# Kernel tuning notes

Measured on AMD Instinct MI355X. Metric: run time of the kernel, lower is better.

## Reference

```python
import jax, jax.numpy as jnp
import numpy as np

N = 16384
E = 262144
HID = 128
NFILT = 128
NGAUSS = 50
NINTER = 6
CUTOFF = 10.0
NUMZ = 100
LOG2 = 0.6931471805599453


def ssp(x):
    # ShiftedSoftplus
    return jax.nn.softplus(x) - LOG2


def setup_inputs() -> dict:
    key = jax.random.key(0)
    ks = jax.random.split(key, 20)
    z = jax.random.randint(ks[0], (N,), 0, NUMZ)
    pos = jax.random.uniform(ks[1], (N, 3), dtype=jnp.float32) * 5.0  # box side 5 -> all pairs < cutoff
    edge_index = jax.random.randint(ks[2], (2, E), 0, N)
    s = lambda k, shape, fan: jax.random.normal(k, shape, dtype=jnp.float32) / np.sqrt(fan)
    params = dict(
        emb=s(ks[3], (NUMZ, HID), 1.0),
        Wf1=s(ks[4], (NINTER, NGAUSS, NFILT), NGAUSS), bf1=jnp.zeros((NINTER, NFILT), jnp.float32),
        Wf2=s(ks[5], (NINTER, NFILT, NFILT), NFILT), bf2=jnp.zeros((NINTER, NFILT), jnp.float32),
        Wl1=s(ks[6], (NINTER, HID, NFILT), HID),
        Wl2=s(ks[7], (NINTER, NFILT, HID), NFILT), bl2=jnp.zeros((NINTER, HID), jnp.float32),
        Wl=s(ks[8], (NINTER, HID, HID), HID), bl=jnp.zeros((NINTER, HID), jnp.float32),
        Wo1=s(ks[9], (HID, HID // 2), HID), bo1=jnp.zeros((HID // 2,), jnp.float32),
        Wo2=s(ks[10], (HID // 2, 1), HID // 2), bo2=jnp.zeros((1,), jnp.float32),
    )
    return dict(z=z, pos=pos, edge_index=edge_index, **params)


def reference(z, pos, edge_index, emb, Wf1, bf1, Wf2, bf2, Wl1, Wl2, bl2, Wl, bl, Wo1, bo1, Wo2, bo2):
    src, dst = edge_index[0], edge_index[1]
    # edge distances and Gaussian smearing
    d = jnp.linalg.norm(pos[src] - pos[dst], axis=-1)          # [E]
    offset = jnp.linspace(0.0, CUTOFF, NGAUSS, dtype=jnp.float32)
    coeff = -0.5 / (offset[1] - offset[0]) ** 2
    ea = jnp.exp(coeff * (d[:, None] - offset) ** 2)            # [E, NGAUSS]
    C = 0.5 * (jnp.cos(d * (np.pi / CUTOFF)) + 1.0)             # cosine cutoff [E]

    h = emb[z]                                                  # [N, HID]
    for i in range(NINTER):
        # continuous-filter weights
        Wfilt = (ssp(ea @ Wf1[i] + bf1[i]) @ Wf2[i] + bf2[i]) * C[:, None]  # [E, NFILT]
        x = h @ Wl1[i]                                          # lin1, no bias [N, NFILT]
        msg = x[src] * Wfilt                                    # gather + filter
        agg = jax.ops.segment_sum(msg, dst, num_segments=N)     # scatter-sum [N, NFILT]
        x = ssp(agg @ Wl2[i] + bl2[i]) @ Wl[i] + bl[i]          # lin2 -> ssp -> lin
        h = h + x

    h = ssp(h @ Wo1 + bo1) @ Wo2 + bo2                          # [N, 1] per-atom energy
    out = jnp.sum(h, axis=0, keepdims=True)                     # 'add' readout, single graph -> [1, 1]
    return jax.nn.relu(out)
```

## Files before the change

kernel.cpp:

```cpp
#include <hip/hip_runtime.h>
#include <math.h>

#define NATOM 16384
#define NEDGE 262144
#define HID 128
#define NG 50
#define NI 6

typedef _Float16 h8_t __attribute__((ext_vector_type(8)));
typedef _Float16 h4_t __attribute__((ext_vector_type(4)));
typedef float    f4_t __attribute__((ext_vector_type(4)));

__device__ __forceinline__ float ssp_f(float v) {
    float e = __expf(-fabsf(v));
    return fmaxf(v, 0.0f) + __logf(1.0f + e) - 0.69314718055994531f;
}

__global__ void fill0(float* __restrict__ p, int n4) {
    int i = blockIdx.x * 256 + threadIdx.x;
    if (i < n4) ((float4*)p)[i] = make_float4(0.f, 0.f, 0.f, 0.f);
}

__global__ void hist_k(const int* __restrict__ ei, int* __restrict__ cnt) {
    int e = blockIdx.x * 256 + threadIdx.x;
    if (e < NEDGE) atomicAdd(&cnt[ei[NEDGE + e]], 1);
}

__global__ void scan_k(const int* __restrict__ cnt, int* __restrict__ offs) {
    __shared__ int part[256];
    int t = threadIdx.x;
    int base = t * 64;
    int s = 0;
    for (int i = 0; i < 64; ++i) s += cnt[base + i];
    part[t] = s;
    __syncthreads();
    for (int off = 1; off < 256; off <<= 1) {
        int v = (t >= off) ? part[t - off] : 0;
        __syncthreads();
        part[t] += v;
        __syncthreads();
    }
    int r = part[t] - s;
    for (int i = 0; i < 64; ++i) { offs[base + i] = r; r += cnt[base + i]; }
    if (t == 255) offs[NATOM] = r;
}

__global__ void scatter_k(const int* __restrict__ ei, const int* __restrict__ offs,
                          int* __restrict__ cnt, int* __restrict__ sSrc, int* __restrict__ sDst) {
    int e = blockIdx.x * 256 + threadIdx.x;
    if (e >= NEDGE) return;
    int d = ei[NEDGE + e];
    int r = atomicAdd(&cnt[d], 1);
    int j = offs[d] + r;
    sSrc[j] = ei[e];
    sDst[j] = d;
}

__global__ void edge_pre(const float* __restrict__ pos,
                         const int* __restrict__ sSrc, const int* __restrict__ sDst,
                         _Float16* __restrict__ eaH, _Float16* __restrict__ eaL,
                         float* __restrict__ Cb) {
    int j = blockIdx.x * 256 + threadIdx.x;
    if (j >= NEDGE) return;
    int s = sSrc[j], dd = sDst[j];
    float dx = pos[3*s]   - pos[3*dd];
    float dy = pos[3*s+1] - pos[3*dd+1];
    float dz = pos[3*s+2] - pos[3*dd+2];
    float d = sqrtf(dx*dx + dy*dy + dz*dz);
    Cb[j] = 0.5f * (cosf(d * 0.31415926535897931f) + 1.0f);
    const float delta = 10.0f / 49.0f;
    const float coeff = -0.5f / (delta * delta);
    #pragma unroll
    for (int gq = 0; gq < 8; ++gq) {
        h8_t hv, lv;
        #pragma unroll
        for (int r = 0; r < 8; ++r) {
            int g = gq * 8 + r;
            float v = 0.0f;
            if (g < NG) { float u = d - (float)g * delta; v = __expf(coeff * u * u); }
            _Float16 hh = (_Float16)v;
            hv[r] = hh;
            lv[r] = (_Float16)(v - (float)hh);
        }
        *(h8_t*)&eaH[(size_t)j * 64 + gq * 8] = hv;
        *(h8_t*)&eaL[(size_t)j * 64 + gq * 8] = lv;
    }
}

__global__ void wprep(const float* __restrict__ Wf1, const float* __restrict__ Wf2,
                      const float* __restrict__ Wl1, const float* __restrict__ Wl2,
                      const float* __restrict__ Wl,
                      _Float16* __restrict__ w1h, _Float16* __restrict__ w1l,
                      _Float16* __restrict__ w2h, _Float16* __restrict__ w2l,
                      _Float16* __restrict__ wnh, _Float16* __restrict__ wnl) {
    int idx = blockIdx.x * 256 + threadIdx.x;
    const int S1 = NI * 128 * 64, S2 = NI * 128 * 128;
    if (idx < S1) {
        int i = idx >> 13, r = idx & 8191, fo = r >> 6, k = r & 63;
        float v = (k < NG) ? Wf1[(size_t)i * NG * 128 + k * 128 + fo] : 0.0f;
        _Float16 hh = (_Float16)v;
        w1h[idx] = hh; w1l[idx] = (_Float16)(v - (float)hh);
        return;
    }
    idx -= S1;
    if (idx < S2) {
        int i = idx >> 14, r = idx & 16383, fo = r >> 7, k = r & 127;
        float v = Wf2[(size_t)i * 128 * 128 + k * 128 + fo];
        _Float16 hh = (_Float16)v;
        w2h[idx] = hh; w2l[idx] = (_Float16)(v - (float)hh);
        return;
    }
    idx -= S2;
    if (idx < 3 * S2) {
        int mi = idx >> 14;
        int r = idx & 16383, fo = r >> 7, k = r & 127;
        int m = mi / NI, i = mi % NI;
        const float* W = (m == 0) ? Wl1 : (m == 1) ? Wl2 : Wl;
        float v = W[(size_t)i * 128 * 128 + k * 128 + fo];
        _Float16 hh = (_Float16)v;
        wnh[idx] = hh; wnl[idx] = (_Float16)(v - (float)hh);
    }
}

__global__ void embed_k(const int* __restrict__ z, const float* __restrict__ emb,
                        float* __restrict__ h) {
    int tid = blockIdx.x * 256 + threadIdx.x;
    int n = tid >> 7, f = tid & 127;
    h[tid] = emb[z[n] * HID + f];
}

__launch_bounds__(256)
__global__ void gemm_node_mfma(const float* __restrict__ A,
                               const _Float16* __restrict__ wth, const _Float16* __restrict__ wtl,
                               float* __restrict__ Cout) {
    __shared__ _Float16 aH[64 * 136];
    __shared__ _Float16 aL[64 * 136];
    int t = threadIdx.x;
    int mb = blockIdx.x * 64;
    #pragma unroll
    for (int j = 0; j < 8; ++j) {
        int idx = t + j * 256;
        int row = idx >> 5, c4 = idx & 31;
        f4_t v = *(const f4_t*)&A[(size_t)(mb + row) * HID + c4 * 4];
        h4_t hh, ll;
        #pragma unroll
        for (int r = 0; r < 4; ++r) {
            _Float16 hx = (_Float16)v[r];
            hh[r] = hx; ll[r] = (_Float16)(v[r] - (float)hx);
        }
        *(h4_t*)&aH[row * 136 + c4 * 4] = hh;
        *(h4_t*)&aL[row * 136 + c4 * 4] = ll;
    }
    __syncthreads();

    int wv = t >> 6, lane = t & 63, l15 = lane & 15, quad = lane >> 4;
    f4_t acc[2][4];
    #pragma unroll
    for (int m = 0; m < 2; ++m)
        #pragma unroll
        for (int n = 0; n < 4; ++n) acc[m][n] = (f4_t)0.0f;

    for (int kc = 0; kc < 4; ++kc) {
        int k0 = kc * 32 + quad * 8;
        h8_t a_h[2], a_l[2];
        #pragma unroll
        for (int m = 0; m < 2; ++m) {
            int fr = wv * 32 + m * 16 + l15;
            a_h[m] = *(const h8_t*)&wth[fr * 128 + k0];
            a_l[m] = *(const h8_t*)&wtl[fr * 128 + k0];
        }
        #pragma unroll
        for (int n = 0; n < 4; ++n) {
            int er = n * 16 + l15;
            h8_t b_h = *(const h8_t*)&aH[er * 136 + k0];
            h8_t b_l = *(const h8_t*)&aL[er * 136 + k0];
            #pragma unroll
            for (int m = 0; m < 2; ++m) {
                acc[m][n] = __builtin_amdgcn_mfma_f32_16x16x32_f16(a_h[m], b_h, acc[m][n], 0, 0, 0);
                acc[m][n] = __builtin_amdgcn_mfma_f32_16x16x32_f16(a_h[m], b_l, acc[m][n], 0, 0, 0);
                acc[m][n] = __builtin_amdgcn_mfma_f32_16x16x32_f16(a_l[m], b_h, acc[m][n], 0, 0, 0);
            }
        }
    }

    #pragma unroll
    for (int n = 0; n < 4; ++n) {
        int el = n * 16 + l15;
        size_t row = (size_t)(mb + el);
        #pragma unroll
        for (int m = 0; m < 2; ++m) {
            int fb = wv * 32 + m * 16 + quad * 4;
            f4_t o;
            #pragma unroll
            for (int r = 0; r < 4; ++r) o[r] = acc[m][n][r];
            *(f4_t*)&Cout[row * 128 + fb] = o;
        }
    }
}

__launch_bounds__(256)
__global__ void gemm_node3(const float* __restrict__ agg,
                           const _Float16* __restrict__ w2th, const _Float16* __restrict__ w2tl,
                           const _Float16* __restrict__ wlth, const _Float16* __restrict__ wltl,
                           const _Float16* __restrict__ w1nh, const _Float16* __restrict__ w1nl,
                           const float* __restrict__ bl2, const float* __restrict__ bl,
                           float* __restrict__ h, float* __restrict__ x) {
    __shared__ _Float16 aH[64 * 136];
    __shared__ _Float16 aL[64 * 136];
    int t = threadIdx.x;
    int mb = blockIdx.x * 64;
    #pragma unroll
    for (int j = 0; j < 8; ++j) {
        int idx = t + j * 256;
        int row = idx >> 5, c4 = idx & 31;
        f4_t v = *(const f4_t*)&agg[(size_t)(mb + row) * HID + c4 * 4];
        h4_t hh, ll;
        #pragma unroll
        for (int r = 0; r < 4; ++r) {
            _Float16 hx = (_Float16)v[r];
            hh[r] = hx; ll[r] = (_Float16)(v[r] - (float)hx);
        }
        *(h4_t*)&aH[row * 136 + c4 * 4] = hh;
        *(h4_t*)&aL[row * 136 + c4 * 4] = ll;
    }
    __syncthreads();

    int wv = t >> 6, lane = t & 63, l15 = lane & 15, quad = lane >> 4;
    int fq = wv * 32 + quad * 4;
    f4_t acc[2][4];

    #pragma unroll
    for (int m = 0; m < 2; ++m)
        #pragma unroll
        for (int n = 0; n < 4; ++n) acc[m][n] = (f4_t)0.0f;
    for (int kc = 0; kc < 4; ++kc) {
        int k0 = kc * 32 + quad * 8;
        h8_t a_h[2], a_l[2];
        #pragma unroll
        for (int m = 0; m < 2; ++m) {
            int fr = wv * 32 + m * 16 + l15;
            a_h[m] = *(const h8_t*)&w2th[fr * 128 + k0];
            a_l[m] = *(const h8_t*)&w2tl[fr * 128 + k0];
        }
        #pragma unroll
        for (int n = 0; n < 4; ++n) {
            int er = n * 16 + l15;
            h8_t b_h = *(const h8_t*)&aH[er * 136 + k0];
            h8_t b_l = *(const h8_t*)&aL[er * 136 + k0];
            #pragma unroll
            for (int m = 0; m < 2; ++m) {
                acc[m][n] = __builtin_amdgcn_mfma_f32_16x16x32_f16(a_h[m], b_h, acc[m][n], 0, 0, 0);
                acc[m][n] = __builtin_amdgcn_mfma_f32_16x16x32_f16(a_h[m], b_l, acc[m][n], 0, 0, 0);
                acc[m][n] = __builtin_amdgcn_mfma_f32_16x16x32_f16(a_l[m], b_h, acc[m][n], 0, 0, 0);
            }
        }
    }
    f4_t b2v[2];
    b2v[0] = *(const f4_t*)&bl2[fq]; b2v[1] = *(const f4_t*)&bl2[fq + 16];
    __syncthreads();

    #pragma unroll
    for (int m = 0; m < 2; ++m)
        #pragma unroll
        for (int n = 0; n < 4; ++n) {
            int el = n * 16 + l15;
            int fb = wv * 32 + m * 16 + quad * 4;
            h4_t hh, ll;
            #pragma unroll
            for (int r = 0; r < 4; ++r) {
                float sv = ssp_f(acc[m][n][r] + b2v[m][r]);
                _Float16 hx = (_Float16)sv;
                hh[r] = hx;
                ll[r] = (_Float16)(sv - (float)hx);
            }
            *(h4_t*)&aH[el * 136 + fb] = hh;
            *(h4_t*)&aL[el * 136 + fb] = ll;
        }
    __syncthreads();

    #pragma unroll
    for (int m = 0; m < 2; ++m)
        #pragma unroll
        for (int n = 0; n < 4; ++n) acc[m][n] = (f4_t)0.0f;
    for (int kc = 0; kc < 4; ++kc) {
        int k0 = kc * 32 + quad * 8;
        h8_t a_h[2], a_l[2];
        #pragma unroll
        for (int m = 0; m < 2; ++m) {
            int fr = wv * 32 + m * 16 + l15;
            a_h[m] = *(const h8_t*)&wlth[fr * 128 + k0];
            a_l[m] = *(const h8_t*)&wltl[fr * 128 + k0];
        }
        #pragma unroll
        for (int n = 0; n < 4; ++n) {
            int er = n * 16 + l15;
            h8_t b_h = *(const h8_t*)&aH[er * 136 + k0];
            h8_t b_l = *(const h8_t*)&aL[er * 136 + k0];
            #pragma unroll
            for (int m = 0; m < 2; ++m) {
                acc[m][n] = __builtin_amdgcn_mfma_f32_16x16x32_f16(a_h[m], b_h, acc[m][n], 0, 0, 0);
                acc[m][n] = __builtin_amdgcn_mfma_f32_16x16x32_f16(a_h[m], b_l, acc[m][n], 0, 0, 0);
                acc[m][n] = __builtin_amdgcn_mfma_f32_16x16x32_f16(a_l[m], b_h, acc[m][n], 0, 0, 0);
            }
        }
    }
    f4_t blv[2];
    blv[0] = *(const f4_t*)&bl[fq]; blv[1] = *(const f4_t*)&bl[fq + 16];
    __syncthreads();

    #pragma unroll
    for (int n = 0; n < 4; ++n) {
        int el = n * 16 + l15;
        size_t row = (size_t)(mb + el);
        #pragma unroll
        for (int m = 0; m < 2; ++m) {
            int fb = wv * 32 + m * 16 + quad * 4;
            f4_t hv = *(const f4_t*)&h[row * 128 + fb];
            f4_t o;
            h4_t hh, ll;
            #pragma unroll
            for (int r = 0; r < 4; ++r) {
                o[r] = hv[r] + acc[m][n][r] + blv[m][r];
                _Float16 hx = (_Float16)o[r];
                hh[r] = hx; ll[r] = (_Float16)(o[r] - (float)hx);
            }
            *(f4_t*)&h[row * 128 + fb] = o;
            *(h4_t*)&aH[el * 136 + fb] = hh;
            *(h4_t*)&aL[el * 136 + fb] = ll;
        }
    }
    if (!w1nh) return;
    __syncthreads();

    #pragma unroll
    for (int m = 0; m < 2; ++m)
        #pragma unroll
        for (int n = 0; n < 4; ++n) acc[m][n] = (f4_t)0.0f;
    for (int kc = 0; kc < 4; ++kc) {
        int k0 = kc * 32 + quad * 8;
        h8_t a_h[2], a_l[2];
        #pragma unroll
        for (int m = 0; m < 2; ++m) {
            int fr = wv * 32 + m * 16 + l15;
            a_h[m] = *(const h8_t*)&w1nh[fr * 128 + k0];
            a_l[m] = *(const h8_t*)&w1nl[fr * 128 + k0];
        }
        #pragma unroll
        for (int n = 0; n < 4; ++n) {
            int er = n * 16 + l15;
            h8_t b_h = *(const h8_t*)&aH[er * 136 + k0];
            h8_t b_l = *(const h8_t*)&aL[er * 136 + k0];
            #pragma unroll
            for (int m = 0; m < 2; ++m) {
                acc[m][n] = __builtin_amdgcn_mfma_f32_16x16x32_f16(a_h[m], b_h, acc[m][n], 0, 0, 0);
                acc[m][n] = __builtin_amdgcn_mfma_f32_16x16x32_f16(a_h[m], b_l, acc[m][n], 0, 0, 0);
                acc[m][n] = __builtin_amdgcn_mfma_f32_16x16x32_f16(a_l[m], b_h, acc[m][n], 0, 0, 0);
            }
        }
    }
    #pragma unroll
    for (int n = 0; n < 4; ++n) {
        int el = n * 16 + l15;
        size_t row = (size_t)(mb + el);
        #pragma unroll
        for (int m = 0; m < 2; ++m) {
            int fb = wv * 32 + m * 16 + quad * 4;
            f4_t o;
            #pragma unroll
            for (int r = 0; r < 4; ++r) o[r] = acc[m][n][r];
            *(f4_t*)&x[row * 128 + fb] = o;
        }
    }
}

#define T1_LDW 136
#define MROW 132
#define EF_TPB 4

__launch_bounds__(256, 2)
__global__ void edge_filter(const float* __restrict__ x, float* __restrict__ agg,
                            const int* __restrict__ sSrc, const int* __restrict__ sDst,
                            const float* __restrict__ Cb,
                            const _Float16* __restrict__ eaH, const _Float16* __restrict__ eaL,
                            const _Float16* __restrict__ w1h, const _Float16* __restrict__ w1l,
                            const _Float16* __restrict__ w2h, const _Float16* __restrict__ w2l,
                            const float* __restrict__ bf1, const float* __restrict__ bf2) {
    __shared__ __align__(16) _Float16 eaHs[64 * 72];
    __shared__ __align__(16) _Float16 eaLs[64 * 72];
    __shared__ __align__(16) unsigned char t1mem[34816];
    __shared__ float cL[64];
    __shared__ int dstl[64];
    __shared__ int srcl[64];

    _Float16* t1H = (_Float16*)t1mem;
    _Float16* t1L = (_Float16*)(t1mem + 17408);
    float*    msg = (float*)t1mem;

    int t = threadIdx.x;
    int wv = t >> 6, lane = t & 63;
    int l15 = lane & 15, quad = lane >> 4;
    int tile0 = blockIdx.x * EF_TPB;

    h8_t w1fh[2][2], w1fl[2][2], w2fh[4][2], w2fl[4][2];
    #pragma unroll
    for (int kc = 0; kc < 2; ++kc) {
        int k0 = kc * 32 + quad * 8;
        #pragma unroll
        for (int m = 0; m < 2; ++m) {
            int fr = wv * 32 + m * 16 + l15;
            w1fh[kc][m] = *(const h8_t*)&w1h[fr * 64 + k0];
            w1fl[kc][m] = *(const h8_t*)&w1l[fr * 64 + k0];
        }
    }
    #pragma unroll
    for (int kc = 0; kc < 4; ++kc) {
        int k0 = kc * 32 + quad * 8;
        #pragma unroll
        for (int m = 0; m < 2; ++m) {
            int fr = wv * 32 + m * 16 + l15;
            w2fh[kc][m] = *(const h8_t*)&w2h[fr * 128 + k0];
            w2fl[kc][m] = *(const h8_t*)&w2l[fr * 128 + k0];
        }
    }
    int fq = wv * 32 + quad * 4;
    f4_t b1v[2], b2v[2];
    b1v[0] = *(const f4_t*)&bf1[fq];  b1v[1] = *(const f4_t*)&bf1[fq + 16];
    b2v[0] = *(const f4_t*)&bf2[fq];  b2v[1] = *(const f4_t*)&bf2[fq + 16];

    {
        int eb = tile0 * 64;
        if (t < 64) {
            srcl[t] = sSrc[eb + t];
            dstl[t] = sDst[eb + t];
            cL[t]   = Cb[eb + t];
        }
        #pragma unroll
        for (int c = 0; c < 4; ++c) {
            int ch = t + c * 256;
            int pl = ch >> 9, rem = ch & 511, e = rem >> 3, ks = rem & 7;
            h8_t v = *(const h8_t*)((pl ? eaL : eaH) + (size_t)(eb + e) * 64 + ks * 8);
            *(h8_t*)((pl ? eaLs : eaHs) + e * 72 + ks * 8) = v;
        }
    }
    __syncthreads();

    for (int tt = 0; tt < EF_TPB; ++tt) {
        if (tt > 0) {
            __syncthreads();
            if (t < 64) {
                int e = (tile0 + tt) * 64 + t;
                srcl[t] = sSrc[e];
                dstl[t] = sDst[e];
                cL[t]   = Cb[e];
            }
        }
        bool pre = (tt < EF_TPB - 1);
        h8_t sreg[4];
        if (pre) {
            int ebn = (tile0 + tt + 1) * 64;
            #pragma unroll
            for (int c = 0; c < 4; ++c) {
                int ch = t + c * 256;
                int pl = ch >> 9, rem = ch & 511, e = rem >> 3, ks = rem & 7;
                sreg[c] = *(const h8_t*)((pl ? eaL : eaH) + (size_t)(ebn + e) * 64 + ks * 8);
            }
        }

        f4_t acc1[2][4];
        #pragma unroll
        for (int m = 0; m < 2; ++m)
            #pragma unroll
            for (int n = 0; n < 4; ++n) acc1[m][n] = (f4_t)0.0f;
        #pragma unroll
        for (int kc = 0; kc < 2; ++kc) {
            int k0 = kc * 32 + quad * 8;
            h8_t b_h[4], b_l[4];
            #pragma unroll
            for (int n = 0; n < 4; ++n) {
                int er = n * 16 + l15;
                b_h[n] = *(const h8_t*)&eaHs[er * 72 + k0];
                b_l[n] = *(const h8_t*)&eaLs[er * 72 + k0];
            }
            #pragma unroll
            for (int m = 0; m < 2; ++m)
                #pragma unroll
                for (int n = 0; n < 4; ++n) {
                    acc1[m][n] = __builtin_amdgcn_mfma_f32_16x16x32_f16(w1fh[kc][m], b_h[n], acc1[m][n], 0, 0, 0);
                    acc1[m][n] = __builtin_amdgcn_mfma_f32_16x16x32_f16(w1fh[kc][m], b_l[n], acc1[m][n], 0, 0, 0);
                    acc1[m][n] = __builtin_amdgcn_mfma_f32_16x16x32_f16(w1fl[kc][m], b_h[n], acc1[m][n], 0, 0, 0);
                }
        }

        #pragma unroll
        for (int m = 0; m < 2; ++m)
            #pragma unroll
            for (int n = 0; n < 4; ++n) {
                int el = n * 16 + l15;
                int fb = wv * 32 + m * 16 + quad * 4;
                h4_t hh, ll;
                #pragma unroll
                for (int r = 0; r < 4; ++r) {
                    float sv = ssp_f(acc1[m][n][r] + b1v[m][r]);
                    _Float16 hx = (_Float16)sv;
                    hh[r] = hx;
                    ll[r] = (_Float16)(sv - (float)hx);
                }
                *(h4_t*)&t1H[el * T1_LDW + fb] = hh;
                *(h4_t*)&t1L[el * T1_LDW + fb] = ll;
            }
        __syncthreads();

        if (pre) {
            #pragma unroll
            for (int c = 0; c < 4; ++c) {
                int ch = t + c * 256;
                int pl = ch >> 9, rem = ch & 511, e = rem >> 3, ks = rem & 7;
                *(h8_t*)((pl ? eaLs : eaHs) + e * 72 + ks * 8) = sreg[c];
            }
        }
        f4_t xr[4][2];
        #pragma unroll
        for (int n = 0; n < 4; ++n) {
            int el = n * 16 + l15;
            int s = srcl[el];
            #pragma unroll
            for (int m = 0; m < 2; ++m) {
                int fb = wv * 32 + m * 16 + quad * 4;
                xr[n][m] = *(const f4_t*)&x[(size_t)s * HID + fb];
            }
        }

        f4_t acc2[2][4];
        #pragma unroll
        for (int m = 0; m < 2; ++m)
            #pragma unroll
            for (int n = 0; n < 4; ++n) acc2[m][n] = (f4_t)0.0f;
        #pragma unroll
        for (int kc = 0; kc < 4; ++kc) {
            int k0 = kc * 32 + quad * 8;
            #pragma unroll
            for (int n = 0; n < 4; ++n) {
                int er = n * 16 + l15;
                h8_t b_h = *(const h8_t*)&t1H[er * T1_LDW + k0];
                h8_t b_l = *(const h8_t*)&t1L[er * T1_LDW + k0];
                #pragma unroll
                for (int m = 0; m < 2; ++m) {
                    acc2[m][n] = __builtin_amdgcn_mfma_f32_16x16x32_f16(w2fh[kc][m], b_h, acc2[m][n], 0, 0, 0);
                    acc2[m][n] = __builtin_amdgcn_mfma_f32_16x16x32_f16(w2fh[kc][m], b_l, acc2[m][n], 0, 0, 0);
                    acc2[m][n] = __builtin_amdgcn_mfma_f32_16x16x32_f16(w2fl[kc][m], b_h, acc2[m][n], 0, 0, 0);
                }
            }
        }
        __syncthreads();

        #pragma unroll
        for (int n = 0; n < 4; ++n) {
            int el = n * 16 + l15;
            float ce = cL[el];
            #pragma unroll
            for (int m = 0; m < 2; ++m) {
                int fb = wv * 32 + m * 16 + quad * 4;
                f4_t o;
                #pragma unroll
                for (int r = 0; r < 4; ++r)
                    o[r] = (acc2[m][n][r] + b2v[m][r]) * ce * xr[n][m][r];
                *(f4_t*)&msg[el * MROW + fb] = o;
            }
        }
        __syncthreads();

        int f = t & 127, hf = t >> 7;
        int ib = hf * 32;
        float run = 0.0f;
        int cur = dstl[ib];
        for (int i = ib; i < ib + 32; ++i) {
            int dnow = dstl[i];
            if (dnow != cur) {
                atomicAdd(&agg[(size_t)cur * HID + f], run);
                run = 0.0f;
                cur = dnow;
            }
            run += msg[i * MROW + f];
        }
        atomicAdd(&agg[(size_t)cur * HID + f], run);
    }
}

__launch_bounds__(256)
__global__ void readout1(const float* __restrict__ h, const float* __restrict__ Wo1,
                         const float* __restrict__ bo1, const float* __restrict__ Wo2,
                         const float* __restrict__ bo2, float* __restrict__ accum) {
    __shared__ float w1[128 * 64];
    __shared__ float part[4];
    int t = threadIdx.x;
    for (int i = t; i < 128 * 16; i += 256)
        ((float4*)w1)[i] = ((const float4*)Wo1)[i];
    __syncthreads();
    int f = t & 63, wv = t >> 6;
    float b = bo1[f], w2v = Wo2[f];
    float lsum = 0.0f;
    for (int a = 0; a < 16; ++a) {
        int n = blockIdx.x * 64 + wv * 16 + a;
        const float* hr = &h[(size_t)n * HID];
        float acc = b;
        #pragma unroll 16
        for (int k = 0; k < 128; ++k)
            acc = fmaf(hr[k], w1[k*64 + f], acc);
        lsum += ssp_f(acc) * w2v;
    }
    #pragma unroll
    for (int off = 32; off > 0; off >>= 1)
        lsum += __shfl_down(lsum, off, 64);
    if (f == 0) part[wv] = lsum;
    __syncthreads();
    if (t == 0)
        atomicAdd(accum, part[0] + part[1] + part[2] + part[3] + 64.0f * bo2[0]);
}

__global__ void readout2(const float* __restrict__ accum, float* __restrict__ out) {
    out[0] = fmaxf(accum[0], 0.0f);
}

extern "C" void kernel_launch(void* const* d_in, const int* in_sizes, int n_in,
                              void* d_out, int out_size, void* d_ws, size_t ws_size,
                              hipStream_t stream) {
    const int*   z   = (const int*)d_in[0];
    const float* pos = (const float*)d_in[1];
    const int*   ei  = (const int*)d_in[2];
    const float* emb = (const float*)d_in[3];
    const float* Wf1 = (const float*)d_in[4];
    const float* bf1 = (const float*)d_in[5];
    const float* Wf2 = (const float*)d_in[6];
    const float* bf2 = (const float*)d_in[7];
    const float* Wl1 = (const float*)d_in[8];
    const float* Wl2 = (const float*)d_in[9];
    const float* bl2 = (const float*)d_in[10];
    const float* Wl  = (const float*)d_in[11];
    const float* bl  = (const float*)d_in[12];
    const float* Wo1 = (const float*)d_in[13];
    const float* bo1 = (const float*)d_in[14];
    const float* Wo2 = (const float*)d_in[15];
    const float* bo2 = (const float*)d_in[16];
    float* out = (float*)d_out;

    _Float16* w1h = (_Float16*)d_ws;
    _Float16* w1l = w1h + NI * 8192;
    _Float16* w2h = w1l + NI * 8192;
    _Float16* w2l = w2h + NI * 16384;
    _Float16* wnh = w2l + NI * 16384;
    _Float16* wnl = wnh + 3 * NI * 16384;
    _Float16* eaH = wnl + 3 * NI * 16384;
    _Float16* eaL = eaH + (size_t)NEDGE * 64;
    float* Cb  = (float*)(eaL + (size_t)NEDGE * 64);
    float* h   = Cb + NEDGE;
    float* x   = h   + (size_t)NATOM * HID;
    float* agg = x   + (size_t)NATOM * HID;
    float* accum = agg + (size_t)NATOM * HID;
    int* cnt  = (int*)(accum + 4);
    int* offs = cnt + NATOM;
    int* sSrc = offs + NATOM + 4;
    int* sDst = sSrc + NEDGE;

    fill0<<<NATOM/4/256, 256, 0, stream>>>((float*)cnt, NATOM/4);
    hist_k<<<NEDGE/256, 256, 0, stream>>>(ei, cnt);
    scan_k<<<1, 256, 0, stream>>>(cnt, offs);
    fill0<<<NATOM/4/256, 256, 0, stream>>>((float*)cnt, NATOM/4);
    scatter_k<<<NEDGE/256, 256, 0, stream>>>(ei, offs, cnt, sSrc, sDst);

    edge_pre<<<NEDGE/256, 256, 0, stream>>>(pos, sSrc, sDst, eaH, eaL, Cb);
    wprep<<<(NI*8192 + NI*16384 + 3*NI*16384)/256, 256, 0, stream>>>(
        Wf1, Wf2, Wl1, Wl2, Wl, w1h, w1l, w2h, w2l, wnh, wnl);
    embed_k<<<(NATOM*HID)/256, 256, 0, stream>>>(z, emb, h);

    gemm_node_mfma<<<256, 256, 0, stream>>>(h, wnh + (size_t)0*16384,
        wnl + (size_t)0*16384, x);
    for (int i = 0; i < NI; ++i) {
        fill0<<<(NATOM*HID/4)/256, 256, 0, stream>>>(agg, NATOM*HID/4);
        edge_filter<<<NEDGE/64/EF_TPB, 256, 0, stream>>>(x, agg, sSrc, sDst, Cb, eaH, eaL,
            w1h + (size_t)i*8192, w1l + (size_t)i*8192,
            w2h + (size_t)i*16384, w2l + (size_t)i*16384,
            bf1 + i*HID, bf2 + i*HID);
        const _Float16* w1nh = (i < NI-1) ? wnh + (size_t)(i+1)*16384 : nullptr;
        const _Float16* w1nl = (i < NI-1) ? wnl + (size_t)(i+1)*16384 : nullptr;
        gemm_node3<<<256, 256, 0, stream>>>(agg,
            wnh + (size_t)(1*NI+i)*16384, wnl + (size_t)(1*NI+i)*16384,
            wnh + (size_t)(2*NI+i)*16384, wnl + (size_t)(2*NI+i)*16384,
            w1nh, w1nl, bl2 + i*HID, bl + i*HID, h, x);
    }
    fill0<<<1, 256, 0, stream>>>(accum, 1);
    readout1<<<NATOM/64, 256, 0, stream>>>(h, Wo1, bo1, Wo2, bo2, accum);
    readout2<<<1, 1, 0, stream>>>(accum, out);
}
```

Before: 791.3 us.

## Use single fp16 edge filter GEMMs, fp16 node features, and register-level segmented scatter

Drops the split hi/lo fp16 emulation of fp32 in the edge filter MLP, so each GEMM uses one MFMA per product instead of three. Node features x are now stored as fp16, halving the gather traffic. The scatter-sum moves from an LDS message buffer with a serial run-length loop to a wave-level segmented scan with shuffles, and edge indices now live in registers. LDS use shrinks and occupancy is raised to 3 blocks per SM. The cost is lower numerical precision in the filter weights and messages, which may break accuracy tolerance.

```diff
diff --git a/kernel.cpp b/kernel.cpp
--- a/kernel.cpp
+++ b/kernel.cpp
@@ -58,8 +58,7 @@
 
 __global__ void edge_pre(const float* __restrict__ pos,
                          const int* __restrict__ sSrc, const int* __restrict__ sDst,
-                         _Float16* __restrict__ eaH, _Float16* __restrict__ eaL,
-                         float* __restrict__ Cb) {
+                         _Float16* __restrict__ ea, float* __restrict__ Cb) {
     int j = blockIdx.x * 256 + threadIdx.x;
     if (j >= NEDGE) return;
     int s = sSrc[j], dd = sDst[j];
@@ -72,42 +71,35 @@
     const float coeff = -0.5f / (delta * delta);
     #pragma unroll
     for (int gq = 0; gq < 8; ++gq) {
-        h8_t hv, lv;
+        h8_t hv;
         #pragma unroll
         for (int r = 0; r < 8; ++r) {
             int g = gq * 8 + r;
             float v = 0.0f;
             if (g < NG) { float u = d - (float)g * delta; v = __expf(coeff * u * u); }
-            _Float16 hh = (_Float16)v;
-            hv[r] = hh;
-            lv[r] = (_Float16)(v - (float)hh);
-        }
-        *(h8_t*)&eaH[(size_t)j * 64 + gq * 8] = hv;
-        *(h8_t*)&eaL[(size_t)j * 64 + gq * 8] = lv;
+            hv[r] = (_Float16)v;
+        }
+        *(h8_t*)&ea[(size_t)j * 64 + gq * 8] = hv;
     }
 }
 
 __global__ void wprep(const float* __restrict__ Wf1, const float* __restrict__ Wf2,
                       const float* __restrict__ Wl1, const float* __restrict__ Wl2,
                       const float* __restrict__ Wl,
-                      _Float16* __restrict__ w1h, _Float16* __restrict__ w1l,
-                      _Float16* __restrict__ w2h, _Float16* __restrict__ w2l,
+                      _Float16* __restrict__ w1, _Float16* __restrict__ w2,
                       _Float16* __restrict__ wnh, _Float16* __restrict__ wnl) {
     int idx = blockIdx.x * 256 + threadIdx.x;
     const int S1 = NI * 128 * 64, S2 = NI * 128 * 128;
     if (idx < S1) {
         int i = idx >> 13, r = idx & 8191, fo = r >> 6, k = r & 63;
         float v = (k < NG) ? Wf1[(size_t)i * NG * 128 + k * 128 + fo] : 0.0f;
-        _Float16 hh = (_Float16)v;
-        w1h[idx] = hh; w1l[idx] = (_Float16)(v - (float)hh);
+        w1[idx] = (_Float16)v;
         return;
     }
     idx -= S1;
     if (idx < S2) {
         int i = idx >> 14, r = idx & 16383, fo = r >> 7, k = r & 127;
-        float v = Wf2[(size_t)i * 128 * 128 + k * 128 + fo];
-        _Float16 hh = (_Float16)v;
-        w2h[idx] = hh; w2l[idx] = (_Float16)(v - (float)hh);
+        w2[idx] = (_Float16)Wf2[(size_t)i * 128 * 128 + k * 128 + fo];
         return;
     }
     idx -= S2;
@@ -132,7 +124,7 @@
 __launch_bounds__(256)
 __global__ void gemm_node_mfma(const float* __restrict__ A,
                                const _Float16* __restrict__ wth, const _Float16* __restrict__ wtl,
-                               float* __restrict__ Cout) {
+                               _Float16* __restrict__ xh) {
     __shared__ _Float16 aH[64 * 136];
     __shared__ _Float16 aL[64 * 136];
     int t = threadIdx.x;
@@ -190,10 +182,10 @@
         #pragma unroll
         for (int m = 0; m < 2; ++m) {
             int fb = wv * 32 + m * 16 + quad * 4;
-            f4_t o;
-            #pragma unroll
-            for (int r = 0; r < 4; ++r) o[r] = acc[m][n][r];
-            *(f4_t*)&Cout[row * 128 + fb] = o;
+            h4_t o;
+            #pragma unroll
+            for (int r = 0; r < 4; ++r) o[r] = (_Float16)acc[m][n][r];
+            *(h4_t*)&xh[row * 128 + fb] = o;
         }
     }
 }
@@ -204,7 +196,7 @@
                            const _Float16* __restrict__ wlth, const _Float16* __restrict__ wltl,
                            const _Float16* __restrict__ w1nh, const _Float16* __restrict__ w1nl,
                            const float* __restrict__ bl2, const float* __restrict__ bl,
-                           float* __restrict__ h, float* __restrict__ x) {
+                           float* __restrict__ h, _Float16* __restrict__ xh) {
     __shared__ _Float16 aH[64 * 136];
     __shared__ _Float16 aL[64 * 136];
     int t = threadIdx.x;
@@ -365,51 +357,41 @@
         #pragma unroll
         for (int m = 0; m < 2; ++m) {
             int fb = wv * 32 + m * 16 + quad * 4;
-            f4_t o;
-            #pragma unroll
-            for (int r = 0; r < 4; ++r) o[r] = acc[m][n][r];
-            *(f4_t*)&x[row * 128 + fb] = o;
+            h4_t o;
+            #pragma unroll
+            for (int r = 0; r < 4; ++r) o[r] = (_Float16)acc[m][n][r];
+            *(h4_t*)&xh[row * 128 + fb] = o;
         }
     }
 }
 
 #define T1_LDW 136
-#define MROW 132
+#define EA_LDW 72
 #define EF_TPB 4
 
-__launch_bounds__(256, 2)
-__global__ void edge_filter(const float* __restrict__ x, float* __restrict__ agg,
+__launch_bounds__(256, 3)
+__global__ void edge_filter(const _Float16* __restrict__ xh, float* __restrict__ agg,
                             const int* __restrict__ sSrc, const int* __restrict__ sDst,
                             const float* __restrict__ Cb,
-                            const _Float16* __restrict__ eaH, const _Float16* __restrict__ eaL,
-                            const _Float16* __restrict__ w1h, const _Float16* __restrict__ w1l,
-                            const _Float16* __restrict__ w2h, const _Float16* __restrict__ w2l,
+                            const _Float16* __restrict__ ea,
+                            const _Float16* __restrict__ w1, const _Float16* __restrict__ w2,
                             const float* __restrict__ bf1, const float* __restrict__ bf2) {
-    __shared__ __align__(16) _Float16 eaHs[64 * 72];
-    __shared__ __align__(16) _Float16 eaLs[64 * 72];
-    __shared__ __align__(16) unsigned char t1mem[34816];
-    __shared__ float cL[64];
-    __shared__ int dstl[64];
-    __shared__ int srcl[64];
-
-    _Float16* t1H = (_Float16*)t1mem;
-    _Float16* t1L = (_Float16*)(t1mem + 17408);
-    float*    msg = (float*)t1mem;
+    __shared__ __align__(16) _Float16 eaS[64 * EA_LDW];
+    __shared__ __align__(16) _Float16 t1S[64 * T1_LDW];
 
     int t = threadIdx.x;
     int wv = t >> 6, lane = t & 63;
     int l15 = lane & 15, quad = lane >> 4;
     int tile0 = blockIdx.x * EF_TPB;
 
-    h8_t w1fh[2][2], w1fl[2][2], w2fh[4][2], w2fl[4][2];
+    h8_t w1f[2][2], w2f[4][2];
     #pragma unroll
     for (int kc = 0; kc < 2; ++kc) {
         int k0 = kc * 32 + quad * 8;
         #pragma unroll
         for (int m = 0; m < 2; ++m) {
             int fr = wv * 32 + m * 16 + l15;
-            w1fh[kc][m] = *(const h8_t*)&w1h[fr * 64 + k0];
-            w1fl[kc][m] = *(const h8_t*)&w1l[fr * 64 + k0];
+            w1f[kc][m] = *(const h8_t*)&w1[fr * 64 + k0];
         }
     }
     #pragma unroll
@@ -418,8 +400,7 @@
         #pragma unroll
         for (int m = 0; m < 2; ++m) {
             int fr = wv * 32 + m * 16 + l15;
-            w2fh[kc][m] = *(const h8_t*)&w2h[fr * 128 + k0];
-            w2fl[kc][m] = *(const h8_t*)&w2l[fr * 128 + k0];
+            w2f[kc][m] = *(const h8_t*)&w2[fr * 128 + k0];
         }
     }
     int fq = wv * 32 + quad * 4;
@@ -427,42 +408,45 @@
     b1v[0] = *(const f4_t*)&bf1[fq];  b1v[1] = *(const f4_t*)&bf1[fq + 16];
     b2v[0] = *(const f4_t*)&bf2[fq];  b2v[1] = *(const f4_t*)&bf2[fq + 16];
 
+    int srcn[4], dstn[4];
+    float cn[4];
     {
         int eb = tile0 * 64;
-        if (t < 64) {
-            srcl[t] = sSrc[eb + t];
-            dstl[t] = sDst[eb + t];
-            cL[t]   = Cb[eb + t];
-        }
-        #pragma unroll
-        for (int c = 0; c < 4; ++c) {
+        #pragma unroll
+        for (int n = 0; n < 4; ++n) {
+            int ge = eb + n * 16 + l15;
+            srcn[n] = sSrc[ge];
+            dstn[n] = sDst[ge];
+            cn[n]   = Cb[ge];
+        }
+        #pragma unroll
+        for (int c = 0; c < 2; ++c) {
             int ch = t + c * 256;
-            int pl = ch >> 9, rem = ch & 511, e = rem >> 3, ks = rem & 7;
-            h8_t v = *(const h8_t*)((pl ? eaL : eaH) + (size_t)(eb + e) * 64 + ks * 8);
-            *(h8_t*)((pl ? eaLs : eaHs) + e * 72 + ks * 8) = v;
+            int e = ch >> 3, ks = ch & 7;
+            *(h8_t*)&eaS[e * EA_LDW + ks * 8] = *(const h8_t*)&ea[(size_t)(eb + e) * 64 + ks * 8];
         }
     }
     __syncthreads();
 
     for (int tt = 0; tt < EF_TPB; ++tt) {
-        if (tt > 0) {
-            __syncthreads();
-            if (t < 64) {
-                int e = (tile0 + tt) * 64 + t;
-                srcl[t] = sSrc[e];
-                dstl[t] = sDst[e];
-                cL[t]   = Cb[e];
-            }
-        }
         bool pre = (tt < EF_TPB - 1);
-        h8_t sreg[4];
+        h8_t sreg[2];
+        int srcp[4], dstp[4];
+        float cp[4];
         if (pre) {
             int ebn = (tile0 + tt + 1) * 64;
             #pragma unroll
-            for (int c = 0; c < 4; ++c) {
+            for (int c = 0; c < 2; ++c) {
                 int ch = t + c * 256;
-                int pl = ch >> 9, rem = ch & 511, e = rem >> 3, ks = rem & 7;
-                sreg[c] = *(const h8_t*)((pl ? eaL : eaH) + (size_t)(ebn + e) * 64 + ks * 8);
+                int e = ch >> 3, ks = ch & 7;
+                sreg[c] = *(const h8_t*)&ea[(size_t)(ebn + e) * 64 + ks * 8];
+            }
+            #pragma unroll
+            for (int n = 0; n < 4; ++n) {
+                int ge = ebn + n * 16 + l15;
+                srcp[n] = sSrc[ge];
+                dstp[n] = sDst[ge];
+                cp[n]   = Cb[ge];
             }
         }
 
@@ -474,21 +458,15 @@
         #pragma unroll
         for (int kc = 0; kc < 2; ++kc) {
             int k0 = kc * 32 + quad * 8;
-            h8_t b_h[4], b_l[4];
-            #pragma unroll
-            for (int n = 0; n < 4; ++n) {
-                int er = n * 16 + l15;
-                b_h[n] = *(const h8_t*)&eaHs[er * 72 + k0];
-                b_l[n] = *(const h8_t*)&eaLs[er * 72 + k0];
-            }
+            h8_t b[4];
+            #pragma unroll
+            for (int n = 0; n < 4; ++n)
+                b[n] = *(const h8_t*)&eaS[(n * 16 + l15) * EA_LDW + k0];
             #pragma unroll
             for (int m = 0; m < 2; ++m)
                 #pragma unroll
-                for (int n = 0; n < 4; ++n) {
-                    acc1[m][n] = __builtin_amdgcn_mfma_f32_16x16x32_f16(w1fh[kc][m], b_h[n], acc1[m][n], 0, 0, 0);
-                    acc1[m][n] = __builtin_amdgcn_mfma_f32_16x16x32_f16(w1fh[kc][m], b_l[n], acc1[m][n], 0, 0, 0);
-                    acc1[m][n] = __builtin_amdgcn_mfma_f32_16x16x32_f16(w1fl[kc][m], b_h[n], acc1[m][n], 0, 0, 0);
-                }
+                for (int n = 0; n < 4; ++n)
+                    acc1[m][n] = __builtin_amdgcn_mfma_f32_16x16x32_f16(w1f[kc][m], b[n], acc1[m][n], 0, 0, 0);
         }
 
         #pragma unroll
@@ -497,92 +475,81 @@
             for (int n = 0; n < 4; ++n) {
                 int el = n * 16 + l15;
                 int fb = wv * 32 + m * 16 + quad * 4;
-                h4_t hh, ll;
+                h4_t hh;
+                #pragma unroll
+                for (int r = 0; r < 4; ++r)
+                    hh[r] = (_Float16)ssp_f(acc1[m][n][r] + b1v[m][r]);
+                *(h4_t*)&t1S[el * T1_LDW + fb] = hh;
+            }
+        __syncthreads();
+
+        if (pre) {
+            #pragma unroll
+            for (int c = 0; c < 2; ++c) {
+                int ch = t + c * 256;
+                int e = ch >> 3, ks = ch & 7;
+                *(h8_t*)&eaS[e * EA_LDW + ks * 8] = sreg[c];
+            }
+        }
+        h4_t xr[4][2];
+        #pragma unroll
+        for (int n = 0; n < 4; ++n) {
+            #pragma unroll
+            for (int m = 0; m < 2; ++m) {
+                int fb = wv * 32 + m * 16 + quad * 4;
+                xr[n][m] = *(const h4_t*)&xh[(size_t)srcn[n] * HID + fb];
+            }
+        }
+
+        f4_t acc2[2][4];
+        #pragma unroll
+        for (int m = 0; m < 2; ++m)
+            #pragma unroll
+            for (int n = 0; n < 4; ++n) acc2[m][n] = (f4_t)0.0f;
+        #pragma unroll
+        for (int kc = 0; kc < 4; ++kc) {
+            int k0 = kc * 32 + quad * 8;
+            #pragma unroll
+            for (int n = 0; n < 4; ++n) {
+                h8_t b = *(const h8_t*)&t1S[(n * 16 + l15) * T1_LDW + k0];
+                #pragma unroll
+                for (int m = 0; m < 2; ++m)
+                    acc2[m][n] = __builtin_amdgcn_mfma_f32_16x16x32_f16(w2f[kc][m], b, acc2[m][n], 0, 0, 0);
+            }
+        }
+        __syncthreads();
+
+        #pragma unroll
+        for (int n = 0; n < 4; ++n) {
+            int dn = dstn[n];
+            int dprev = __shfl_up(dn, 1, 16);
+            int dnext = __shfl_down(dn, 1, 16);
+            bool head = (l15 == 0) || (dn != dprev);
+            bool tail = (l15 == 15) || (dn != dnext);
+            unsigned long long bb = __ballot(head);
+            unsigned grp = (unsigned)(bb >> (quad * 16)) & 0xFFFFu;
+            unsigned le = grp & ((2u << l15) - 1u);
+            int myStart = 31 - __builtin_clz(le);
+            float ce = cn[n];
+            #pragma unroll
+            for (int m = 0; m < 2; ++m) {
+                int fb = wv * 32 + m * 16 + quad * 4;
                 #pragma unroll
                 for (int r = 0; r < 4; ++r) {
-                    float sv = ssp_f(acc1[m][n][r] + b1v[m][r]);
-                    _Float16 hx = (_Float16)sv;
-                    hh[r] = hx;
-                    ll[r] = (_Float16)(sv - (float)hx);
+                    float o = (acc2[m][n][r] + b2v[m][r]) * ce * (float)xr[n][m][r];
+                    #pragma unroll
+                    for (int d = 1; d < 16; d <<= 1) {
+                        float u = __shfl_up(o, d, 16);
+                        o += ((int)l15 - d >= myStart) ? u : 0.0f;
+                    }
+                    if (tail) atomicAdd(&agg[(size_t)dn * HID + fb + r], o);
                 }
-                *(h4_t*)&t1H[el * T1_LDW + fb] = hh;
-                *(h4_t*)&t1L[el * T1_LDW + fb] = ll;
-            }
-        __syncthreads();
-
+            }
+        }
         if (pre) {
             #pragma unroll
-            for (int c = 0; c < 4; ++c) {
-                int ch = t + c * 256;
-                int pl = ch >> 9, rem = ch & 511, e = rem >> 3, ks = rem & 7;
-                *(h8_t*)((pl ? eaLs : eaHs) + e * 72 + ks * 8) = sreg[c];
-            }
-        }
-        f4_t xr[4][2];
-        #pragma unroll
-        for (int n = 0; n < 4; ++n) {
-            int el = n * 16 + l15;
-            int s = srcl[el];
-            #pragma unroll
-            for (int m = 0; m < 2; ++m) {
-                int fb = wv * 32 + m * 16 + quad * 4;
-                xr[n][m] = *(const f4_t*)&x[(size_t)s * HID + fb];
-            }
-        }
-
-        f4_t acc2[2][4];
-        #pragma unroll
-        for (int m = 0; m < 2; ++m)
-            #pragma unroll
-            for (int n = 0; n < 4; ++n) acc2[m][n] = (f4_t)0.0f;
-        #pragma unroll
-        for (int kc = 0; kc < 4; ++kc) {
-            int k0 = kc * 32 + quad * 8;
-            #pragma unroll
-            for (int n = 0; n < 4; ++n) {
-                int er = n * 16 + l15;
-                h8_t b_h = *(const h8_t*)&t1H[er * T1_LDW + k0];
-                h8_t b_l = *(const h8_t*)&t1L[er * T1_LDW + k0];
-                #pragma unroll
-                for (int m = 0; m < 2; ++m) {
-                    acc2[m][n] = __builtin_amdgcn_mfma_f32_16x16x32_f16(w2fh[kc][m], b_h, acc2[m][n], 0, 0, 0);
-                    acc2[m][n] = __builtin_amdgcn_mfma_f32_16x16x32_f16(w2fh[kc][m], b_l, acc2[m][n], 0, 0, 0);
-                    acc2[m][n] = __builtin_amdgcn_mfma_f32_16x16x32_f16(w2fl[kc][m], b_h, acc2[m][n], 0, 0, 0);
-                }
-            }
-        }
-        __syncthreads();
-
-        #pragma unroll
-        for (int n = 0; n < 4; ++n) {
-            int el = n * 16 + l15;
-            float ce = cL[el];
-            #pragma unroll
-            for (int m = 0; m < 2; ++m) {
-                int fb = wv * 32 + m * 16 + quad * 4;
-                f4_t o;
-                #pragma unroll
-                for (int r = 0; r < 4; ++r)
-                    o[r] = (acc2[m][n][r] + b2v[m][r]) * ce * xr[n][m][r];
-                *(f4_t*)&msg[el * MROW + fb] = o;
-            }
-        }
-        __syncthreads();
-
-        int f = t & 127, hf = t >> 7;
-        int ib = hf * 32;
-        float run = 0.0f;
-        int cur = dstl[ib];
-        for (int i = ib; i < ib + 32; ++i) {
-            int dnow = dstl[i];
-            if (dnow != cur) {
-                atomicAdd(&agg[(size_t)cur * HID + f], run);
-                run = 0.0f;
-                cur = dnow;
-            }
-            run += msg[i * MROW + f];
-        }
-        atomicAdd(&agg[(size_t)cur * HID + f], run);
+            for (int n = 0; n < 4; ++n) { srcn[n] = srcp[n]; dstn[n] = dstp[n]; cn[n] = cp[n]; }
+        }
     }
 }
 
@@ -643,18 +610,15 @@
     const float* bo2 = (const float*)d_in[16];
     float* out = (float*)d_out;
 
-    _Float16* w1h = (_Float16*)d_ws;
-    _Float16* w1l = w1h + NI * 8192;
-    _Float16* w2h = w1l + NI * 8192;
-    _Float16* w2l = w2h + NI * 16384;
-    _Float16* wnh = w2l + NI * 16384;
+    _Float16* w1  = (_Float16*)d_ws;
+    _Float16* w2  = w1 + NI * 8192;
+    _Float16* wnh = w2 + NI * 16384;
     _Float16* wnl = wnh + 3 * NI * 16384;
-    _Float16* eaH = wnl + 3 * NI * 16384;
-    _Float16* eaL = eaH + (size_t)NEDGE * 64;
-    float* Cb  = (float*)(eaL + (size_t)NEDGE * 64);
+    _Float16* ea  = wnl + 3 * NI * 16384;
+    _Float16* xh  = ea + (size_t)NEDGE * 64;
+    float* Cb  = (float*)(xh + (size_t)NATOM * 128);
     float* h   = Cb + NEDGE;
-    float* x   = h   + (size_t)NATOM * HID;
-    float* agg = x   + (size_t)NATOM * HID;
+    float* agg = h + (size_t)NATOM * HID;
     float* accum = agg + (size_t)NATOM * HID;
     int* cnt  = (int*)(accum + 4);
     int* offs = cnt + NATOM;
@@ -667,25 +631,24 @@
     fill0<<<NATOM/4/256, 256, 0, stream>>>((float*)cnt, NATOM/4);
     scatter_k<<<NEDGE/256, 256, 0, stream>>>(ei, offs, cnt, sSrc, sDst);
 
-    edge_pre<<<NEDGE/256, 256, 0, stream>>>(pos, sSrc, sDst, eaH, eaL, Cb);
+    edge_pre<<<NEDGE/256, 256, 0, stream>>>(pos, sSrc, sDst, ea, Cb);
     wprep<<<(NI*8192 + NI*16384 + 3*NI*16384)/256, 256, 0, stream>>>(
-        Wf1, Wf2, Wl1, Wl2, Wl, w1h, w1l, w2h, w2l, wnh, wnl);
+        Wf1, Wf2, Wl1, Wl2, Wl, w1, w2, wnh, wnl);
     embed_k<<<(NATOM*HID)/256, 256, 0, stream>>>(z, emb, h);
 
     gemm_node_mfma<<<256, 256, 0, stream>>>(h, wnh + (size_t)0*16384,
-        wnl + (size_t)0*16384, x);
+        wnl + (size_t)0*16384, xh);
     for (int i = 0; i < NI; ++i) {
         fill0<<<(NATOM*HID/4)/256, 256, 0, stream>>>(agg, NATOM*HID/4);
-        edge_filter<<<NEDGE/64/EF_TPB, 256, 0, stream>>>(x, agg, sSrc, sDst, Cb, eaH, eaL,
-            w1h + (size_t)i*8192, w1l + (size_t)i*8192,
-            w2h + (size_t)i*16384, w2l + (size_t)i*16384,
+        edge_filter<<<NEDGE/64/EF_TPB, 256, 0, stream>>>(xh, agg, sSrc, sDst, Cb, ea,
+            w1 + (size_t)i*8192, w2 + (size_t)i*16384,
             bf1 + i*HID, bf2 + i*HID);
         const _Float16* w1nh = (i < NI-1) ? wnh + (size_t)(i+1)*16384 : nullptr;
         const _Float16* w1nl = (i < NI-1) ? wnl + (size_t)(i+1)*16384 : nullptr;
         gemm_node3<<<256, 256, 0, stream>>>(agg,
             wnh + (size_t)(1*NI+i)*16384, wnl + (size_t)(1*NI+i)*16384,
             wnh + (size_t)(2*NI+i)*16384, wnl + (size_t)(2*NI+i)*16384,
-            w1nh, w1nl, bl2 + i*HID, bl + i*HID, h, x);
+            w1nh, w1nl, bl2 + i*HID, bl + i*HID, h, xh);
     }
     fill0<<<1, 256, 0, stream>>>(accum, 1);
     readout1<<<NATOM/64, 256, 0, stream>>>(h, Wo1, bo1, Wo2, bo2, accum);
```

New measurement: 1.026 ms. 1.3x slower.
